# Performance work log

Measured on AMD Instinct MI355X. Metric: run time of the kernel, lower is better.

## Reference

```python
import jax, jax.numpy as jnp
import numpy as np

B, C, H, W = 16, 256, 32, 32
AD, SC, R = 16, 32, 4


def _conv1x1(x, w, b):
    # x: [B,Cin,H,W], w: [Cout,Cin], b: [Cout]
    return jnp.einsum('oc,bchw->bohw', w, x) + b[None, :, None, None]


def setup_inputs() -> dict:
    key = jax.random.key(0)
    ks = jax.random.split(key, 12)
    p = lambda k, shape: (jax.random.normal(k, shape, dtype=jnp.float32) * 0.02)
    return {
        'x': jax.random.normal(ks[0], (B, C, H, W), dtype=jnp.float32),
        'fc1_w': p(ks[1], (C // R, C)), 'fc1_b': jnp.zeros((C // R,), jnp.float32),
        'fc2_w': p(ks[2], (C, C // R)), 'fc2_b': jnp.zeros((C,), jnp.float32),
        'qkv_w': p(ks[3], (AD * 2 + SC, SC)), 'qkv_b': jnp.zeros((AD * 2 + SC,), jnp.float32),
        'proj_w': p(ks[4], (SC, SC)), 'proj_b': jnp.zeros((SC,), jnp.float32),
        'ffn1_w': p(ks[5], (4 * C, C)), 'ffn1_b': jnp.zeros((4 * C,), jnp.float32),
        'ffn2_w': p(ks[6], (C, 4 * C)), 'ffn2_b': jnp.zeros((C,), jnp.float32),
    }


def reference(x, fc1_w, fc1_b, fc2_w, fc2_b, qkv_w, qkv_b, proj_w, proj_b,
              ffn1_w, ffn1_b, ffn2_w, ffn2_b):
    # --- DynamicChannelSelect: SE gate then channel split ---
    s = x.mean(axis=(2, 3), keepdims=True)                       # [B,C,1,1]
    s = jax.nn.relu(_conv1x1(s, fc1_w, fc1_b))
    s = jax.nn.sigmoid(_conv1x1(s, fc2_w, fc2_b))
    xg = x * s
    attn_part, non_attn_part = xg[:, :SC], xg[:, SC:]

    # --- SHSA: single-head self-attention on SC channels ---
    qkv = _conv1x1(attn_part, qkv_w, qkv_b)                      # [B,2*AD+SC,H,W]
    q = qkv[:, :AD].reshape(B, AD, H * W)
    k = qkv[:, AD:2 * AD].reshape(B, AD, H * W)
    v = qkv[:, 2 * AD:].reshape(B, SC, H * W)
    scale = AD ** -0.5
    attn = jax.nn.softmax(jnp.einsum('bcn,bcm->bnm', q, k) * scale, axis=-1)  # [B,N,N]
    out = jnp.einsum('bcm,bnm->bcn', v, attn).reshape(B, SC, H, W)
    attn_out = _conv1x1(out, proj_w, proj_b)

    # --- concat + 1x1-conv FFN ---
    y = jnp.concatenate([attn_out, non_attn_part], axis=1)       # [B,C,H,W]
    h = jax.nn.relu(_conv1x1(y, ffn1_w, ffn1_b))                 # [B,4C,H,W]
    return _conv1x1(h, ffn2_w, ffn2_b)                           # [B,C,H,W]
```

## Files before the change

### kernel.cpp

```cpp
#include <hip/hip_runtime.h>
#include <cstdint>
#include <cstddef>

#define BB 16
#define CC 256
#define NP 1024

typedef __attribute__((ext_vector_type(8))) short bf16x8;
typedef __attribute__((ext_vector_type(4))) float f32x4;
typedef unsigned short u16;

__device__ __forceinline__ u16 f2bf(float f) {
    union { float f; uint32_t u; } v; v.f = f;
    uint32_t u = v.u;
    return (u16)((u + 0x7FFFu + ((u >> 16) & 1u)) >> 16);
}

__global__ __launch_bounds__(256)
void se_mean_conv_kernel(const float* __restrict__ x, float* __restrict__ s_mean,
                         const float* __restrict__ w1, u16* __restrict__ d1,
                         const float* __restrict__ w2, u16* __restrict__ d2) {
    int blk = blockIdx.x;
    int t = threadIdx.x;
    if (blk < BB * CC) {
        const float* p = x + (size_t)blk * NP;
        float4 v = *(const float4*)(p + t * 4);
        float s = (v.x + v.y) + (v.z + v.w);
#pragma unroll
        for (int off = 32; off; off >>= 1) s += __shfl_down(s, off, 64);
        __shared__ float red[4];
        if ((t & 63) == 0) red[t >> 6] = s;
        __syncthreads();
        if (t == 0) s_mean[blk] = (red[0] + red[1] + red[2] + red[3]) * (1.0f / NP);
    } else {
        int blk2 = blk - BB * CC;
        const float* src = (blk2 < 256) ? w1 : w2;
        u16* dst = (blk2 < 256) ? d1 : d2;
        int i = ((blk2 & 255) * 256 + t) * 4;
        float4 v = *(const float4*)(src + i);
        ushort4 o;
        o.x = f2bf(v.x); o.y = f2bf(v.y); o.z = f2bf(v.z); o.w = f2bf(v.w);
        *(ushort4*)(dst + i) = o;
    }
}

__global__ __launch_bounds__(256)
void scale_transpose_qkv_kernel(const float* __restrict__ x, const float* __restrict__ s_mean,
                                const float* __restrict__ fc1_w, const float* __restrict__ fc1_b,
                                const float* __restrict__ fc2_w, const float* __restrict__ fc2_b,
                                const float* __restrict__ qW, const float* __restrict__ qB,
                                u16* __restrict__ ygt, u16* __restrict__ Qt,
                                u16* __restrict__ Kt, u16* __restrict__ Vb) {
    int nt = blockIdx.x, ct = blockIdx.y, b = blockIdx.z;
    __shared__ float tile[64][65];
    __shared__ float ws[64 * 32];
    __shared__ float bs[64];
    __shared__ float vtile[32][64];
    __shared__ float smean_s[CC];
    __shared__ float h1[64];
    __shared__ float sig_l[64];
    int t = threadIdx.x;
    const float* Xb = x + ((size_t)b * CC + ct * 64) * NP + nt * 64;
    smean_s[t] = s_mean[b * CC + t];
    if (ct == 0) {
        for (int e = t; e < 2048; e += 256) ws[e] = qW[e];
        if (t < 64) bs[t] = qB[t];
    }
#pragma unroll
    for (int p = 0; p < 4; ++p) {
        int e = t + p * 256;
        int c = e >> 4, n4 = (e & 15) * 4;
        float4 v = *(const float4*)&Xb[(size_t)c * NP + n4];
        tile[c][n4] = v.x; tile[c][n4 + 1] = v.y; tile[c][n4 + 2] = v.z; tile[c][n4 + 3] = v.w;
    }
    __syncthreads();
    if (t < 64) {
        float a = fc1_b[t];
#pragma unroll 4
        for (int c = 0; c < CC; ++c) a += fc1_w[t * CC + c] * smean_s[c];
        h1[t] = fmaxf(a, 0.f);
    }
    __syncthreads();
    if (t < 64) {
        int c = ct * 64 + t;
        float a = fc2_b[c];
#pragma unroll 8
        for (int j = 0; j < 64; ++j) a += fc2_w[c * 64 + j] * h1[j];
        sig_l[t] = 1.f / (1.f + __expf(-a));
    }
    __syncthreads();
    u16* Yb = ygt + ((size_t)b * NP + nt * 64) * CC + ct * 64;
#pragma unroll
    for (int p = 0; p < 4; ++p) {
        int e = t + p * 256;
        int n = e >> 4, c4 = (e & 15) * 4;
        if (ct * 64 + c4 >= 32) {
            ushort4 o;
            o.x = f2bf(tile[c4][n] * sig_l[c4]);
            o.y = f2bf(tile[c4 + 1][n] * sig_l[c4 + 1]);
            o.z = f2bf(tile[c4 + 2][n] * sig_l[c4 + 2]);
            o.w = f2bf(tile[c4 + 3][n] * sig_l[c4 + 3]);
            *(ushort4*)&Yb[(size_t)n * CC + c4] = o;
        }
    }
    if (ct == 0) {
        int nn = t & 63, g = t >> 6;
        int n = nt * 64 + nn;
        float xs[32];
#pragma unroll
        for (int c = 0; c < 32; ++c) xs[c] = tile[c][nn] * sig_l[c];
        float acc[16];
#pragma unroll
        for (int oc = 0; oc < 16; ++oc) {
            int o = g * 16 + oc;
            float a = bs[o];
#pragma unroll
            for (int c = 0; c < 32; ++c) a += ws[o * 32 + c] * xs[c];
            acc[oc] = a;
        }
        if (g == 0) {
            u16* qr = Qt + ((size_t)b * NP + n) * 32;
            ushort4 z4; z4.x = 0; z4.y = 0; z4.z = 0; z4.w = 0;
#pragma unroll
            for (int j = 0; j < 16; j += 4) {
                ushort4 o4;
                o4.x = f2bf(acc[j] * 0.25f);     o4.y = f2bf(acc[j + 1] * 0.25f);
                o4.z = f2bf(acc[j + 2] * 0.25f); o4.w = f2bf(acc[j + 3] * 0.25f);
                *(ushort4*)&qr[j] = o4;
            }
            *(ushort4*)&qr[16] = z4; *(ushort4*)&qr[20] = z4;
            *(ushort4*)&qr[24] = z4; *(ushort4*)&qr[28] = z4;
        } else if (g == 1) {
            u16* kr = Kt + ((size_t)b * NP + n) * 32;
            ushort4 z4; z4.x = 0; z4.y = 0; z4.z = 0; z4.w = 0;
#pragma unroll
            for (int j = 0; j < 16; j += 4) {
                ushort4 k4;
                k4.x = f2bf(acc[j]);     k4.y = f2bf(acc[j + 1]);
                k4.z = f2bf(acc[j + 2]); k4.w = f2bf(acc[j + 3]);
                *(ushort4*)&kr[j] = k4;
            }
            *(ushort4*)&kr[16] = z4; *(ushort4*)&kr[20] = z4;
            *(ushort4*)&kr[24] = z4; *(ushort4*)&kr[28] = z4;
        } else {
#pragma unroll
            for (int oc = 0; oc < 16; ++oc) vtile[(g - 2) * 16 + oc][nn] = acc[oc];
        }
        __syncthreads();
        for (int e = t; e < 2048; e += 256) {
            int c = e >> 6, nn2 = e & 63;
            Vb[(size_t)b * 32 * NP + (size_t)c * NP + nt * 64 + nn2] = f2bf(vtile[c][nn2]);
        }
    }
}

__global__ __launch_bounds__(256)
void attn_mfma_kernel(const u16* __restrict__ Qt, const u16* __restrict__ Kt,
                      const u16* __restrict__ Vb,
                      const float* __restrict__ proj_w, const float* __restrict__ proj_b,
                      u16* __restrict__ ygt) {
    int b = blockIdx.x & 15;
    int n0 = (blockIdx.x >> 4) * 16;
    __shared__ __align__(16) u16 P_lds[4][16][40];
    __shared__ float al_lds[4][16];
    __shared__ float sm_lds[4][16];
    __shared__ float sl_lds[4][16];
    __shared__ float O_lds[4][16][33];
    __shared__ float pw_s[32][32];
    __shared__ float pb_s[32];
    int t = threadIdx.x;
    int w = t >> 6, lane = t & 63;
    int q = lane >> 4, idx = lane & 15;

    for (int e = t; e < 1024; e += 256) pw_s[e >> 5][e & 31] = proj_w[e];
    if (t < 32) pb_s[t] = proj_b[t];
    __syncthreads();

    const u16* Qb = Qt + (size_t)b * NP * 32;
    const u16* Kb = Kt + (size_t)b * NP * 32;
    const u16* Vp = Vb + (size_t)b * 32 * NP;

    int nrow = n0 + idx;
    bf16x8 aq = *(const bf16x8*)&Qb[(size_t)nrow * 32 + q * 8];

    f32x4 O0 = {0.f, 0.f, 0.f, 0.f}, O1 = {0.f, 0.f, 0.f, 0.f};
    float m_run[4] = {-1e30f, -1e30f, -1e30f, -1e30f};
    float l_run[4] = {0.f, 0.f, 0.f, 0.f};

    int mbase = w * 256;
    for (int m0 = mbase; m0 < mbase + 256; m0 += 32) {
        bf16x8 bk0 = *(const bf16x8*)&Kb[(size_t)(m0 + idx) * 32 + q * 8];
        bf16x8 bk1 = *(const bf16x8*)&Kb[(size_t)(m0 + 16 + idx) * 32 + q * 8];
        bf16x8 va0 = *(const bf16x8*)&Vp[(size_t)idx * NP + m0 + q * 8];
        bf16x8 va1 = *(const bf16x8*)&Vp[(size_t)(16 + idx) * NP + m0 + q * 8];
        f32x4 z = {0.f, 0.f, 0.f, 0.f};
        f32x4 S0 = __builtin_amdgcn_mfma_f32_16x16x32_bf16(aq, bk0, z, 0, 0, 0);
        f32x4 S1 = __builtin_amdgcn_mfma_f32_16x16x32_bf16(aq, bk1, z, 0, 0, 0);
        float mx[4], p0[4], p1[4], alpha[4];
#pragma unroll
        for (int r = 0; r < 4; ++r) mx[r] = fmaxf(S0[r], S1[r]);
#pragma unroll
        for (int off = 1; off < 16; off <<= 1)
#pragma unroll
            for (int r = 0; r < 4; ++r) mx[r] = fmaxf(mx[r], __shfl_xor(mx[r], off, 64));
#pragma unroll
        for (int r = 0; r < 4; ++r) {
            float nm = fmaxf(m_run[r], mx[r]);
            alpha[r] = __expf(m_run[r] - nm);
            m_run[r] = nm;
            p0[r] = __expf(S0[r] - nm);
            p1[r] = __expf(S1[r] - nm);
        }
#pragma unroll
        for (int r = 0; r < 4; ++r) {
            float s = p0[r] + p1[r];
#pragma unroll
            for (int off = 1; off < 16; off <<= 1) s += __shfl_xor(s, off, 64);
            l_run[r] = l_run[r] * alpha[r] + s;
        }
#pragma unroll
        for (int r = 0; r < 4; ++r) {
            P_lds[w][q * 4 + r][idx]      = f2bf(p0[r]);
            P_lds[w][q * 4 + r][idx + 16] = f2bf(p1[r]);
        }
        if (idx == 0) {
#pragma unroll
            for (int r = 0; r < 4; ++r) al_lds[w][q * 4 + r] = alpha[r];
        }
        float an = al_lds[w][idx];
#pragma unroll
        for (int r = 0; r < 4; ++r) { O0[r] *= an; O1[r] *= an; }
        bf16x8 pf = *(const bf16x8*)&P_lds[w][idx][q * 8];
        O0 = __builtin_amdgcn_mfma_f32_16x16x32_bf16(va0, pf, O0, 0, 0, 0);
        O1 = __builtin_amdgcn_mfma_f32_16x16x32_bf16(va1, pf, O1, 0, 0, 0);
    }
    if (idx == 0) {
#pragma unroll
        for (int r = 0; r < 4; ++r) {
            sm_lds[w][q * 4 + r] = m_run[r];
            sl_lds[w][q * 4 + r] = l_run[r];
        }
    }
#pragma unroll
    for (int r = 0; r < 4; ++r) {
        O_lds[w][idx][q * 4 + r]      = O0[r];
        O_lds[w][idx][q * 4 + r + 16] = O1[r];
    }
    __syncthreads();
    if (w == 0) {
        float m0_ = sm_lds[0][idx], m1 = sm_lds[1][idx], m2 = sm_lds[2][idx], m3 = sm_lds[3][idx];
        float gm = fmaxf(fmaxf(m0_, m1), fmaxf(m2, m3));
        float e0 = __expf(m0_ - gm), e1 = __expf(m1 - gm);
        float e2 = __expf(m2 - gm), e3 = __expf(m3 - gm);
        float linv = 1.f / (sl_lds[0][idx] * e0 + sl_lds[1][idx] * e1 +
                            sl_lds[2][idx] * e2 + sl_lds[3][idx] * e3);
#pragma unroll
        for (int r = 0; r < 4; ++r) {
            int c0 = q * 4 + r;
            O_lds[0][idx][c0] = (O_lds[0][idx][c0] * e0 + O_lds[1][idx][c0] * e1 +
                                 O_lds[2][idx][c0] * e2 + O_lds[3][idx][c0] * e3) * linv;
            int c1 = c0 + 16;
            O_lds[0][idx][c1] = (O_lds[0][idx][c1] * e0 + O_lds[1][idx][c1] * e1 +
                                 O_lds[2][idx][c1] * e2 + O_lds[3][idx][c1] * e3) * linv;
        }
        float o0[4], o1[4];
#pragma unroll
        for (int r = 0; r < 4; ++r) { o0[r] = pb_s[q * 4 + r]; o1[r] = pb_s[q * 4 + r + 16]; }
#pragma unroll
        for (int c = 0; c < 32; ++c) {
            float xv = O_lds[0][idx][c];
#pragma unroll
            for (int r = 0; r < 4; ++r) {
                o0[r] += pw_s[q * 4 + r][c] * xv;
                o1[r] += pw_s[q * 4 + r + 16][c] * xv;
            }
        }
        u16* yrow = ygt + ((size_t)b * NP + n0 + idx) * CC;
        ushort4 w0, w1;
        w0.x = f2bf(o0[0]); w0.y = f2bf(o0[1]); w0.z = f2bf(o0[2]); w0.w = f2bf(o0[3]);
        w1.x = f2bf(o1[0]); w1.y = f2bf(o1[1]); w1.z = f2bf(o1[2]); w1.w = f2bf(o1[3]);
        *(ushort4*)&yrow[q * 4] = w0;
        *(ushort4*)&yrow[q * 4 + 16] = w1;
    }
}

__global__ __launch_bounds__(256)
void ffn_fused_kernel(const u16* __restrict__ w1b, const u16* __restrict__ w2b,
                      const u16* __restrict__ ygt,
                      const float* __restrict__ bias1, const float* __restrict__ bias2,
                      float* __restrict__ out) {
    __shared__ __align__(16) u16 Ys[4][64][64];
    __shared__ __align__(16) u16 Hs[2][64][64];
    __shared__ float Bs1[1024];
    int t = threadIdx.x;
    int w = t >> 6, lane = t & 63;
    int q = lane >> 4, idx = lane & 15;
    int srow = lane >> 3;
    int gch = (lane & 7) ^ srow;
    int n0 = blockIdx.x * 64;

#pragma unroll
    for (int p = 0; p < 8; ++p) {
        int kb = p >> 1;
        int nb = (p & 1) * 32 + w * 8;
        __builtin_amdgcn_global_load_lds(
            (const __attribute__((address_space(1))) void*)(ygt + (size_t)(n0 + nb + srow) * CC + kb * 64 + gch * 8),
            (__attribute__((address_space(3))) void*)(&Ys[kb][nb][0]),
            16, 0, 0);
    }
    for (int e = t; e < 1024; e += 256) Bs1[e] = bias1[e];

    f32x4 oacc[4][4];
#pragma unroll
    for (int f = 0; f < 4; ++f)
#pragma unroll
        for (int j = 0; j < 4; ++j) { f32x4 z = {0.f, 0.f, 0.f, 0.f}; oacc[f][j] = z; }

    __syncthreads();

    bf16x8 af[8];
    {
        const u16* a1 = w1b + ((size_t)(w * 16 + idx)) * CC;
#pragma unroll
        for (int s = 0; s < 8; ++s) af[s] = *(const bf16x8*)(a1 + s * 32 + q * 8);
    }

    for (int ch = 0; ch < 16; ++ch) {
        bf16x8 af2[4][2];
        const u16* a2 = w2b + ((size_t)(w * 64 + idx)) * 1024 + ch * 64;
#pragma unroll
        for (int f = 0; f < 4; ++f)
#pragma unroll
            for (int s2 = 0; s2 < 2; ++s2)
                af2[f][s2] = *(const bf16x8*)(a2 + (size_t)f * 16 * 1024 + s2 * 32 + q * 8);

        f32x4 hacc[4];
#pragma unroll
        for (int j = 0; j < 4; ++j) { f32x4 z = {0.f, 0.f, 0.f, 0.f}; hacc[j] = z; }
#pragma unroll
        for (int s = 0; s < 8; ++s) {
            int kb = s >> 1, hh = s & 1;
#pragma unroll
            for (int j = 0; j < 4; ++j) {
                bf16x8 yb = *(const bf16x8*)&Ys[kb][j * 16 + idx][(((q + 4 * hh) ^ (idx & 7)) * 8)];
                hacc[j] = __builtin_amdgcn_mfma_f32_16x16x32_bf16(af[s], yb, hacc[j], 0, 0, 0);
            }
        }
        int mbase = ch * 64 + w * 16 + q * 4;
        float b0 = Bs1[mbase], b1v = Bs1[mbase + 1], b2v = Bs1[mbase + 2], b3v = Bs1[mbase + 3];
        int chk_hi = w * 2 + (q >> 1);
#pragma unroll
        for (int j = 0; j < 4; ++j) {
            int n = j * 16 + idx;
            int chk = chk_hi ^ (n & 7);
            uint32_t lo = (uint32_t)f2bf(fmaxf(hacc[j][0] + b0, 0.f)) |
                          ((uint32_t)f2bf(fmaxf(hacc[j][1] + b1v, 0.f)) << 16);
            uint32_t hi = (uint32_t)f2bf(fmaxf(hacc[j][2] + b2v, 0.f)) |
                          ((uint32_t)f2bf(fmaxf(hacc[j][3] + b3v, 0.f)) << 16);
            uint32_t* hp = (uint32_t*)&Hs[ch & 1][n][chk * 8 + (q & 1) * 4];
            hp[0] = lo; hp[1] = hi;
        }
        __syncthreads();
        if (ch + 1 < 16) {
            const u16* a1 = w1b + ((size_t)((ch + 1) * 64 + w * 16 + idx)) * CC;
#pragma unroll
            for (int s = 0; s < 8; ++s) af[s] = *(const bf16x8*)(a1 + s * 32 + q * 8);
        }
#pragma unroll
        for (int s2 = 0; s2 < 2; ++s2)
#pragma unroll
            for (int j = 0; j < 4; ++j) {
                bf16x8 hb = *(const bf16x8*)&Hs[ch & 1][j * 16 + idx][(((q + 4 * s2) ^ (idx & 7)) * 8)];
#pragma unroll
                for (int f = 0; f < 4; ++f)
                    oacc[f][j] = __builtin_amdgcn_mfma_f32_16x16x32_bf16(af2[f][s2], hb, oacc[f][j], 0, 0, 0);
            }
    }

    int b = n0 >> 10, nnb = n0 & 1023;
#pragma unroll
    for (int f = 0; f < 4; ++f) {
        int m2 = w * 64 + f * 16 + q * 4;
        float c0 = bias2[m2], c1 = bias2[m2 + 1], c2 = bias2[m2 + 2], c3 = bias2[m2 + 3];
#pragma unroll
        for (int j = 0; j < 4; ++j) {
            float* p = out + ((size_t)b * CC + m2) * NP + nnb + j * 16 + idx;
            f32x4 v = oacc[f][j];
            p[0]      = v.x + c0;
            p[NP]     = v.y + c1;
            p[2 * NP] = v.z + c2;
            p[3 * NP] = v.w + c3;
        }
    }
}

extern "C" void kernel_launch(void* const* d_in, const int* in_sizes, int n_in,
                              void* d_out, int out_size, void* d_ws, size_t ws_size,
                              hipStream_t stream) {
    const float* x      = (const float*)d_in[0];
    const float* fc1_w  = (const float*)d_in[1];
    const float* fc1_b  = (const float*)d_in[2];
    const float* fc2_w  = (const float*)d_in[3];
    const float* fc2_b  = (const float*)d_in[4];
    const float* qkv_w  = (const float*)d_in[5];
    const float* qkv_b  = (const float*)d_in[6];
    const float* proj_w = (const float*)d_in[7];
    const float* proj_b = (const float*)d_in[8];
    const float* ffn1_w = (const float*)d_in[9];
    const float* ffn1_b = (const float*)d_in[10];
    const float* ffn2_w = (const float*)d_in[11];
    const float* ffn2_b = (const float*)d_in[12];
    float* out = (float*)d_out;

    u16* w1b = (u16*)d_ws;
    u16* w2b = w1b + 262144;
    u16* ygt = w2b + 262144;
    u16* scratch = ygt + (size_t)BB * NP * CC;
    float* s_mean = (float*)scratch;
    u16* Qt = (u16*)(s_mean + BB * CC);
    u16* Kt = Qt + (size_t)BB * NP * 32;
    u16* Vb = Kt + (size_t)BB * NP * 32;

    se_mean_conv_kernel<<<BB * CC + 512, 256, 0, stream>>>(x, s_mean, ffn1_w, w1b, ffn2_w, w2b);
    scale_transpose_qkv_kernel<<<dim3(16, 4, BB), 256, 0, stream>>>(
        x, s_mean, fc1_w, fc1_b, fc2_w, fc2_b, qkv_w, qkv_b, ygt, Qt, Kt, Vb);
    attn_mfma_kernel<<<BB * 64, 256, 0, stream>>>(Qt, Kt, Vb, proj_w, proj_b, ygt);

    ffn_fused_kernel<<<256, 256, 0, stream>>>(w1b, w2b, ygt, ffn1_b, ffn2_b, out);
}
```

Baseline: 172.5 us.

## Hoist SE MLP into separate kernel and halve FFN pixel tile

The SE gate MLP (fc1/relu/fc2/sigmoid), previously recomputed redundantly by every scale/transpose block with 64 serial threads, moves into a small per-batch kernel. That kernel spreads fc1 across all 256 threads and writes sigmoid gates to workspace. The fused FFN kernel now processes 32 pixels per block instead of 64, doubling the grid to 512 blocks to fill more CUs on the MI355X. The cost is an extra launch, and the FFN weight tiles are reloaded twice as often per pixel.

```diff
diff --git a/kernel.cpp b/kernel.cpp
--- a/kernel.cpp
+++ b/kernel.cpp
@@ -45,9 +45,32 @@
 }
 
 __global__ __launch_bounds__(256)
-void scale_transpose_qkv_kernel(const float* __restrict__ x, const float* __restrict__ s_mean,
-                                const float* __restrict__ fc1_w, const float* __restrict__ fc1_b,
-                                const float* __restrict__ fc2_w, const float* __restrict__ fc2_b,
+void se_mlp_kernel(const float* __restrict__ s_mean,
+                   const float* __restrict__ fc1_w, const float* __restrict__ fc1_b,
+                   const float* __restrict__ fc2_w, const float* __restrict__ fc2_b,
+                   float* __restrict__ sig) {
+    int b = blockIdx.x, t = threadIdx.x;
+    __shared__ float sm[256];
+    __shared__ float part[4][64];
+    __shared__ float h1[64];
+    sm[t] = s_mean[b * 256 + t];
+    __syncthreads();
+    int to = t & 63, g = t >> 6;
+    float a = 0.f;
+#pragma unroll 8
+    for (int c = 0; c < 64; ++c) a += fc1_w[to * 256 + g * 64 + c] * sm[g * 64 + c];
+    part[g][to] = a;
+    __syncthreads();
+    if (t < 64) h1[t] = fmaxf(part[0][t] + part[1][t] + part[2][t] + part[3][t] + fc1_b[t], 0.f);
+    __syncthreads();
+    float acc = fc2_b[t];
+#pragma unroll 8
+    for (int j = 0; j < 64; ++j) acc += fc2_w[t * 64 + j] * h1[j];
+    sig[b * 256 + t] = 1.f / (1.f + __expf(-acc));
+}
+
+__global__ __launch_bounds__(256)
+void scale_transpose_qkv_kernel(const float* __restrict__ x, const float* __restrict__ sig,
                                 const float* __restrict__ qW, const float* __restrict__ qB,
                                 u16* __restrict__ ygt, u16* __restrict__ Qt,
                                 u16* __restrict__ Kt, u16* __restrict__ Vb) {
@@ -56,12 +79,10 @@
     __shared__ float ws[64 * 32];
     __shared__ float bs[64];
     __shared__ float vtile[32][64];
-    __shared__ float smean_s[CC];
-    __shared__ float h1[64];
     __shared__ float sig_l[64];
     int t = threadIdx.x;
     const float* Xb = x + ((size_t)b * CC + ct * 64) * NP + nt * 64;
-    smean_s[t] = s_mean[b * CC + t];
+    if (t < 64) sig_l[t] = sig[b * 256 + ct * 64 + t];
     if (ct == 0) {
         for (int e = t; e < 2048; e += 256) ws[e] = qW[e];
         if (t < 64) bs[t] = qB[t];
@@ -72,21 +93,6 @@
         int c = e >> 4, n4 = (e & 15) * 4;
         float4 v = *(const float4*)&Xb[(size_t)c * NP + n4];
         tile[c][n4] = v.x; tile[c][n4 + 1] = v.y; tile[c][n4 + 2] = v.z; tile[c][n4 + 3] = v.w;
-    }
-    __syncthreads();
-    if (t < 64) {
-        float a = fc1_b[t];
-#pragma unroll 4
-        for (int c = 0; c < CC; ++c) a += fc1_w[t * CC + c] * smean_s[c];
-        h1[t] = fmaxf(a, 0.f);
-    }
-    __syncthreads();
-    if (t < 64) {
-        int c = ct * 64 + t;
-        float a = fc2_b[c];
-#pragma unroll 8
-        for (int j = 0; j < 64; ++j) a += fc2_w[c * 64 + j] * h1[j];
-        sig_l[t] = 1.f / (1.f + __expf(-a));
     }
     __syncthreads();
     u16* Yb = ygt + ((size_t)b * NP + nt * 64) * CC + ct * 64;
@@ -289,20 +295,20 @@
                       const u16* __restrict__ ygt,
                       const float* __restrict__ bias1, const float* __restrict__ bias2,
                       float* __restrict__ out) {
-    __shared__ __align__(16) u16 Ys[4][64][64];
-    __shared__ __align__(16) u16 Hs[2][64][64];
+    __shared__ __align__(16) u16 Ys[4][32][64];
+    __shared__ __align__(16) u16 Hs[2][32][64];
     __shared__ float Bs1[1024];
     int t = threadIdx.x;
     int w = t >> 6, lane = t & 63;
     int q = lane >> 4, idx = lane & 15;
     int srow = lane >> 3;
     int gch = (lane & 7) ^ srow;
-    int n0 = blockIdx.x * 64;
-
-#pragma unroll
-    for (int p = 0; p < 8; ++p) {
-        int kb = p >> 1;
-        int nb = (p & 1) * 32 + w * 8;
+    int n0 = blockIdx.x * 32;
+
+#pragma unroll
+    for (int p = 0; p < 4; ++p) {
+        int kb = p;
+        int nb = w * 8;
         __builtin_amdgcn_global_load_lds(
             (const __attribute__((address_space(1))) void*)(ygt + (size_t)(n0 + nb + srow) * CC + kb * 64 + gch * 8),
             (__attribute__((address_space(3))) void*)(&Ys[kb][nb][0]),
@@ -310,11 +316,11 @@
     }
     for (int e = t; e < 1024; e += 256) Bs1[e] = bias1[e];
 
-    f32x4 oacc[4][4];
+    f32x4 oacc[4][2];
 #pragma unroll
     for (int f = 0; f < 4; ++f)
 #pragma unroll
-        for (int j = 0; j < 4; ++j) { f32x4 z = {0.f, 0.f, 0.f, 0.f}; oacc[f][j] = z; }
+        for (int j = 0; j < 2; ++j) { f32x4 z = {0.f, 0.f, 0.f, 0.f}; oacc[f][j] = z; }
 
     __syncthreads();
 
@@ -334,14 +340,14 @@
             for (int s2 = 0; s2 < 2; ++s2)
                 af2[f][s2] = *(const bf16x8*)(a2 + (size_t)f * 16 * 1024 + s2 * 32 + q * 8);
 
-        f32x4 hacc[4];
-#pragma unroll
-        for (int j = 0; j < 4; ++j) { f32x4 z = {0.f, 0.f, 0.f, 0.f}; hacc[j] = z; }
+        f32x4 hacc[2];
+#pragma unroll
+        for (int j = 0; j < 2; ++j) { f32x4 z = {0.f, 0.f, 0.f, 0.f}; hacc[j] = z; }
 #pragma unroll
         for (int s = 0; s < 8; ++s) {
             int kb = s >> 1, hh = s & 1;
 #pragma unroll
-            for (int j = 0; j < 4; ++j) {
+            for (int j = 0; j < 2; ++j) {
                 bf16x8 yb = *(const bf16x8*)&Ys[kb][j * 16 + idx][(((q + 4 * hh) ^ (idx & 7)) * 8)];
                 hacc[j] = __builtin_amdgcn_mfma_f32_16x16x32_bf16(af[s], yb, hacc[j], 0, 0, 0);
             }
@@ -350,7 +356,7 @@
         float b0 = Bs1[mbase], b1v = Bs1[mbase + 1], b2v = Bs1[mbase + 2], b3v = Bs1[mbase + 3];
         int chk_hi = w * 2 + (q >> 1);
 #pragma unroll
-        for (int j = 0; j < 4; ++j) {
+        for (int j = 0; j < 2; ++j) {
             int n = j * 16 + idx;
             int chk = chk_hi ^ (n & 7);
             uint32_t lo = (uint32_t)f2bf(fmaxf(hacc[j][0] + b0, 0.f)) |
@@ -369,7 +375,7 @@
 #pragma unroll
         for (int s2 = 0; s2 < 2; ++s2)
 #pragma unroll
-            for (int j = 0; j < 4; ++j) {
+            for (int j = 0; j < 2; ++j) {
                 bf16x8 hb = *(const bf16x8*)&Hs[ch & 1][j * 16 + idx][(((q + 4 * s2) ^ (idx & 7)) * 8)];
 #pragma unroll
                 for (int f = 0; f < 4; ++f)
@@ -383,7 +389,7 @@
         int m2 = w * 64 + f * 16 + q * 4;
         float c0 = bias2[m2], c1 = bias2[m2 + 1], c2 = bias2[m2 + 2], c3 = bias2[m2 + 3];
 #pragma unroll
-        for (int j = 0; j < 4; ++j) {
+        for (int j = 0; j < 2; ++j) {
             float* p = out + ((size_t)b * CC + m2) * NP + nnb + j * 16 + idx;
             f32x4 v = oacc[f][j];
             p[0]      = v.x + c0;
@@ -417,14 +423,16 @@
     u16* ygt = w2b + 262144;
     u16* scratch = ygt + (size_t)BB * NP * CC;
     float* s_mean = (float*)scratch;
-    u16* Qt = (u16*)(s_mean + BB * CC);
+    float* sig    = s_mean + BB * CC;
+    u16* Qt = (u16*)(sig + BB * CC);
     u16* Kt = Qt + (size_t)BB * NP * 32;
     u16* Vb = Kt + (size_t)BB * NP * 32;
 
     se_mean_conv_kernel<<<BB * CC + 512, 256, 0, stream>>>(x, s_mean, ffn1_w, w1b, ffn2_w, w2b);
+    se_mlp_kernel<<<BB, 256, 0, stream>>>(s_mean, fc1_w, fc1_b, fc2_w, fc2_b, sig);
     scale_transpose_qkv_kernel<<<dim3(16, 4, BB), 256, 0, stream>>>(
-        x, s_mean, fc1_w, fc1_b, fc2_w, fc2_b, qkv_w, qkv_b, ygt, Qt, Kt, Vb);
+        x, sig, qkv_w, qkv_b, ygt, Qt, Kt, Vb);
     attn_mfma_kernel<<<BB * 64, 256, 0, stream>>>(Qt, Kt, Vb, proj_w, proj_b, ygt);
 
-    ffn_fused_kernel<<<256, 256, 0, stream>>>(w1b, w2b, ygt, ffn1_b, ffn2_b, out);
-}
+    ffn_fused_kernel<<<512, 256, 0, stream>>>(w1b, w2b, ygt, ffn1_b, ffn2_b, out);
+}
```

After: 196.7 us. 1.14x slower.
